# Kernel optimization log

Measured on AMD Instinct MI355X. Metric: run time of the kernel, lower is better.

The kernel has to match this reference:

```python
import jax, jax.numpy as jnp
import numpy as np

B, H, SQ, SKV, D = 2, 16, 2048, 3072, 64
NUM_PT = 1024  # SKV = NUM_PT + SQ


def setup_inputs() -> dict:
    key = jax.random.key(0)
    kq, kk, kv = jax.random.split(key, 3)
    q = jax.random.normal(kq, (B, H, SQ, D), dtype=jnp.float32)
    k = jax.random.normal(kk, (B, H, SKV, D), dtype=jnp.float32)
    v = jax.random.normal(kv, (B, H, SKV, D), dtype=jnp.float32)
    return {"q": q, "k": k, "v": v, "num_pt": NUM_PT}


def _prefix_causal_mask(sq, skv, num_pt):
    # kv_idx < num_pt always visible (global prefix); otherwise causal on
    # shifted index: q_idx >= kv_idx - num_pt
    q_idx = jnp.arange(sq)[:, None]   # [SQ,1]
    kv_idx = jnp.arange(skv)[None, :]  # [1,SKV]
    return (kv_idx < num_pt) | (q_idx >= kv_idx - num_pt)  # [SQ,SKV]


def reference(q, k, v, num_pt):
    scale = 1.0 / jnp.sqrt(jnp.asarray(q.shape[-1], q.dtype))
    # [B,H,SQ,SKV]
    scores = jnp.einsum("bhqd,bhkd->bhqk", q, k) * scale
    mask = _prefix_causal_mask(q.shape[2], k.shape[2], num_pt)  # [SQ,SKV]
    neg = jnp.asarray(jnp.finfo(scores.dtype).min, scores.dtype)
    scores = jnp.where(mask[None, None], scores, neg)
    probs = jax.nn.softmax(scores, axis=-1)
    return jnp.einsum("bhqk,bhkd->bhqd", probs, v)
```

## Files before the change

### kernel.cpp

```cpp
#include <hip/hip_runtime.h>

#define B_ 2
#define H_ 16
#define SQ_ 2048
#define SKV_ 3072
#define DH 64
#define QT 128
#define KVT 64
#define LDK 72

typedef __attribute__((ext_vector_type(4))) float f32x4;
typedef __attribute__((ext_vector_type(8))) short bf16x8;

__device__ __forceinline__ unsigned pk2(float a, float b) {
  return __builtin_amdgcn_perm(__float_as_uint(b) + 0x8000u,
                               __float_as_uint(a) + 0x8000u, 0x07060302u);
}

__global__ __launch_bounds__(512, 4) void attn_fwd(
    const float* __restrict__ qg_, const float* __restrict__ kg_,
    const float* __restrict__ vg_, const int* __restrict__ num_pt_p,
    float* __restrict__ og_) {
  __shared__ __align__(16) short Ks[2][KVT][LDK];
  __shared__ __align__(16) short Vt[2][DH][LDK];
  __shared__ __align__(16) short Ps[8][16][LDK];

  const int tid  = (int)threadIdx.x;
  const int lane = tid & 63;
  const int w    = tid >> 6;
  const int lq   = lane & 15;
  const int quad = lane >> 4;
  const int x    = (int)blockIdx.x;
  const int y    = (int)blockIdx.y;
  const int qb   = (y & 16) ? x : (15 - x);
  const int num_pt = *num_pt_p;
  const int q0   = qb * QT;

  const float* qg = qg_ + (size_t)y * SQ_ * DH;
  const float* kg = kg_ + (size_t)y * SKV_ * DH;
  const float* vg = vg_ + (size_t)y * SKV_ * DH;
  float*       og = og_ + (size_t)y * SQ_ * DH;

  const float SC = 0.125f * 1.44269504088896341f;

  const int qrow = q0 + w * 16 + lq;
  bf16x8 qf[2];
  {
    const float* qp = qg + (size_t)qrow * DH + quad * 8;
#pragma unroll
    for (int kh = 0; kh < 2; ++kh) {
      float4 a = *(const float4*)(qp + kh * 32);
      float4 b = *(const float4*)(qp + kh * 32 + 4);
      union { unsigned u[4]; bf16x8 hh; } t;
      t.u[0] = pk2(a.x * SC, a.y * SC);
      t.u[1] = pk2(a.z * SC, a.w * SC);
      t.u[2] = pk2(b.x * SC, b.y * SC);
      t.u[3] = pk2(b.z * SC, b.w * SC);
      qf[kh] = t.hh;
    }
  }

  f32x4 O[4];
#pragma unroll
  for (int i = 0; i < 4; ++i) O[i] = (f32x4){0.f, 0.f, 0.f, 0.f};
  f32x4 l4 = (f32x4){0.f, 0.f, 0.f, 0.f};

  int n_tiles = (q0 + QT - 1 + num_pt) / KVT + 1;
  if (n_tiles > SKV_ / KVT) n_tiles = SKV_ / KVT;

  const int krow = tid >> 3;
  const int kcol = (tid & 7) * 8;
  const int vp   = tid & 31;
  const int vd0  = (tid >> 5) * 4;
  const float* kQp = kg + (size_t)krow * DH + kcol;
  const float* vQp = vg + (size_t)(2 * vp) * DH + vd0;

  float4 kf0 = *(const float4*)(kQp);
  float4 kf1 = *(const float4*)(kQp + 4);
  float4 vfa = *(const float4*)(vQp);
  float4 vfb = *(const float4*)(vQp + DH);

  {
    union { unsigned u[4]; bf16x8 hh; } tk;
    tk.u[0] = pk2(kf0.x, kf0.y);
    tk.u[1] = pk2(kf0.z, kf0.w);
    tk.u[2] = pk2(kf1.x, kf1.y);
    tk.u[3] = pk2(kf1.z, kf1.w);
    *(bf16x8*)&Ks[0][krow][kcol] = tk.hh;
    *(unsigned*)&Vt[0][vd0 + 0][2 * vp] = pk2(vfa.x, vfb.x);
    *(unsigned*)&Vt[0][vd0 + 1][2 * vp] = pk2(vfa.y, vfb.y);
    *(unsigned*)&Vt[0][vd0 + 2][2 * vp] = pk2(vfa.z, vfb.z);
    *(unsigned*)&Vt[0][vd0 + 3][2 * vp] = pk2(vfa.w, vfb.w);
  }
  __syncthreads();

  const int lim = qrow + num_pt;

  for (int t = 0; t < n_tiles; ++t) {
    const int kb = t * KVT;
    const int buf = t & 1;
    const bool more = (t + 1 < n_tiles);

    if (more) {
      const size_t nb = (size_t)(t + 1) * KVT * DH;
      kf0 = *(const float4*)(kQp + nb);
      kf1 = *(const float4*)(kQp + nb + 4);
      vfa = *(const float4*)(vQp + nb);
      vfb = *(const float4*)(vQp + nb + DH);
    }

    f32x4 st[4];
#pragma unroll
    for (int mg = 0; mg < 4; ++mg) {
      bf16x8 ka0 = *(const bf16x8*)&Ks[buf][mg * 16 + lq][quad * 8];
      bf16x8 ka1 = *(const bf16x8*)&Ks[buf][mg * 16 + lq][32 + quad * 8];
      f32x4 c = (f32x4){0.f, 0.f, 0.f, 0.f};
      c = __builtin_amdgcn_mfma_f32_16x16x32_bf16(ka0, qf[0], c, 0, 0, 0);
      c = __builtin_amdgcn_mfma_f32_16x16x32_bf16(ka1, qf[1], c, 0, 0, 0);
      st[mg] = c;
    }

    if (kb + KVT - 1 > q0 + w * 16 + num_pt) {
#pragma unroll
      for (int mg = 0; mg < 4; ++mg)
#pragma unroll
        for (int r = 0; r < 4; ++r)
          if (kb + mg * 16 + quad * 4 + r > lim) st[mg][r] = -__builtin_inff();
    }

#pragma unroll
    for (int mg = 0; mg < 4; ++mg)
#pragma unroll
      for (int r = 0; r < 4; ++r) {
        float pe = __builtin_amdgcn_exp2f(st[mg][r]);
        st[mg][r] = pe;
        l4[r] += pe;
      }

#pragma unroll
    for (int mg = 0; mg < 4; ++mg) {
      *(uint2*)&Ps[w][lq][mg * 16 + quad * 4] =
          make_uint2(pk2(st[mg][0], st[mg][1]), pk2(st[mg][2], st[mg][3]));
    }
    bf16x8 pa0 = *(const bf16x8*)&Ps[w][lq][quad * 8];
    bf16x8 pa1 = *(const bf16x8*)&Ps[w][lq][32 + quad * 8];
#pragma unroll
    for (int dg = 0; dg < 4; ++dg) {
      bf16x8 vb0 = *(const bf16x8*)&Vt[buf][dg * 16 + lq][quad * 8];
      bf16x8 vb1 = *(const bf16x8*)&Vt[buf][dg * 16 + lq][32 + quad * 8];
      O[dg] = __builtin_amdgcn_mfma_f32_16x16x32_bf16(vb0, pa0, O[dg], 0, 0, 0);
      O[dg] = __builtin_amdgcn_mfma_f32_16x16x32_bf16(vb1, pa1, O[dg], 0, 0, 0);
    }

    if (more) {
      union { unsigned u[4]; bf16x8 hh; } tk;
      tk.u[0] = pk2(kf0.x, kf0.y);
      tk.u[1] = pk2(kf0.z, kf0.w);
      tk.u[2] = pk2(kf1.x, kf1.y);
      tk.u[3] = pk2(kf1.z, kf1.w);
      *(bf16x8*)&Ks[buf ^ 1][krow][kcol] = tk.hh;
      *(unsigned*)&Vt[buf ^ 1][vd0 + 0][2 * vp] = pk2(vfa.x, vfb.x);
      *(unsigned*)&Vt[buf ^ 1][vd0 + 1][2 * vp] = pk2(vfa.y, vfb.y);
      *(unsigned*)&Vt[buf ^ 1][vd0 + 2][2 * vp] = pk2(vfa.z, vfb.z);
      *(unsigned*)&Vt[buf ^ 1][vd0 + 3][2 * vp] = pk2(vfa.w, vfb.w);
    }
    __syncthreads();
  }

  float l_run = l4[0] + l4[1] + l4[2] + l4[3];
  l_run += __shfl_xor(l_run, 16);
  l_run += __shfl_xor(l_run, 32);
  float inv = 1.0f / l_run;
  float* op = og + (size_t)qrow * DH + quad * 4;
#pragma unroll
  for (int dg = 0; dg < 4; ++dg) {
    float4 o4;
    o4.x = O[dg][0] * inv;
    o4.y = O[dg][1] * inv;
    o4.z = O[dg][2] * inv;
    o4.w = O[dg][3] * inv;
    *(float4*)(op + dg * 16) = o4;
  }
}

extern "C" void kernel_launch(void* const* d_in, const int* in_sizes, int n_in,
                              void* d_out, int out_size, void* d_ws, size_t ws_size,
                              hipStream_t stream) {
  const float* q = (const float*)d_in[0];
  const float* k = (const float*)d_in[1];
  const float* v = (const float*)d_in[2];
  const int* np  = (const int*)d_in[3];
  float* out = (float*)d_out;
  dim3 grid(SQ_ / QT, B_ * H_);
  attn_fwd<<<grid, dim3(512), 0, stream>>>(q, k, v, np, out);
}
```

Before: 157.7 us.

## Prepack K and transposed V to bf16 in workspace, read fragments directly

Adds a prepass kernel that converts K to bf16 and V to a transposed bf16 layout in the workspace. A new attention kernel with 64-row query tiles and 256 threads loads MFMA fragments straight from global memory into registers, prefetching the next K tile. This removes the LDS staging and the per-tile barriers. It costs an extra kernel launch and a full K/V read and write pass, and it falls back to the old kernel when the workspace is too small.

```diff
diff --git a/kernel.cpp b/kernel.cpp
--- a/kernel.cpp
+++ b/kernel.cpp
@@ -5,7 +5,6 @@
 #define SQ_ 2048
 #define SKV_ 3072
 #define DH 64
-#define QT 128
 #define KVT 64
 #define LDK 72
 
@@ -17,6 +16,189 @@
                                __float_as_uint(a) + 0x8000u, 0x07060302u);
 }
 
+__global__ __launch_bounds__(256) void prepack(
+    const float* __restrict__ kg, const float* __restrict__ vg,
+    short* __restrict__ kb, short* __restrict__ vtb) {
+  const int t = (int)threadIdx.x;
+  const int x = (int)blockIdx.x;
+  const int y = (int)blockIdx.y;
+  if (blockIdx.z == 0) {
+    const float* src = kg + ((size_t)y * SKV_ + (size_t)x * 64) * DH;
+    short* dst = kb + ((size_t)y * SKV_ + (size_t)x * 64) * DH;
+#pragma unroll
+    for (int i = 0; i < 4; ++i) {
+      size_t off = (size_t)i * 1024 + t * 4;
+      float4 f = *(const float4*)(src + off);
+      *(uint2*)(dst + off) = make_uint2(pk2(f.x, f.y), pk2(f.z, f.w));
+    }
+  } else {
+    __shared__ __align__(16) short L[DH][LDK];
+    const float* src = vg + ((size_t)y * SKV_ + (size_t)x * 64) * DH;
+    const int vp = t & 31;
+    const int d0 = (t >> 5) * 8;
+    float4 a0 = *(const float4*)(src + (size_t)(2 * vp) * DH + d0);
+    float4 a1 = *(const float4*)(src + (size_t)(2 * vp) * DH + d0 + 4);
+    float4 b0 = *(const float4*)(src + (size_t)(2 * vp + 1) * DH + d0);
+    float4 b1 = *(const float4*)(src + (size_t)(2 * vp + 1) * DH + d0 + 4);
+    *(unsigned*)&L[d0 + 0][2 * vp] = pk2(a0.x, b0.x);
+    *(unsigned*)&L[d0 + 1][2 * vp] = pk2(a0.y, b0.y);
+    *(unsigned*)&L[d0 + 2][2 * vp] = pk2(a0.z, b0.z);
+    *(unsigned*)&L[d0 + 3][2 * vp] = pk2(a0.w, b0.w);
+    *(unsigned*)&L[d0 + 4][2 * vp] = pk2(a1.x, b1.x);
+    *(unsigned*)&L[d0 + 5][2 * vp] = pk2(a1.y, b1.y);
+    *(unsigned*)&L[d0 + 6][2 * vp] = pk2(a1.z, b1.z);
+    *(unsigned*)&L[d0 + 7][2 * vp] = pk2(a1.w, b1.w);
+    __syncthreads();
+#pragma unroll
+    for (int i = 0; i < 2; ++i) {
+      int cid = t + i * 256;
+      int d = cid >> 3, c = cid & 7;
+      *(bf16x8*)(vtb + ((size_t)y * DH + d) * SKV_ + (size_t)x * 64 + c * 8) =
+          *(const bf16x8*)&L[d][c * 8];
+    }
+  }
+}
+
+__global__ __launch_bounds__(256, 4) void attn_fwd2(
+    const short* __restrict__ kb_, const short* __restrict__ vtb_,
+    const float* __restrict__ qg_, const int* __restrict__ num_pt_p,
+    float* __restrict__ og_) {
+  __shared__ __align__(16) short Ps[4][16][LDK];
+
+  const int tid  = (int)threadIdx.x;
+  const int lane = tid & 63;
+  const int w    = tid >> 6;
+  const int lq   = lane & 15;
+  const int quad = lane >> 4;
+  const int x    = (int)blockIdx.x;
+  const int y    = (int)blockIdx.y;
+  const int g = y >> 3;
+  const int xr = (x + ((g & 2) ? 8 : 0)) & 31;
+  const int qb = (g & 1) ? (31 - xr) : xr;
+  const int num_pt = *num_pt_p;
+  const int q0 = qb * 64;
+
+  const short* Kb = kb_ + (size_t)y * SKV_ * DH;
+  const short* Vb = vtb_ + (size_t)y * DH * SKV_;
+  const float* qg = qg_ + (size_t)y * SQ_ * DH;
+  float*       og = og_ + (size_t)y * SQ_ * DH;
+
+  const float SC = 0.125f * 1.44269504088896341f;
+
+  const int qrow = q0 + w * 16 + lq;
+  bf16x8 qf[2];
+  {
+    const float* qp = qg + (size_t)qrow * DH + quad * 8;
+#pragma unroll
+    for (int kh = 0; kh < 2; ++kh) {
+      float4 a = *(const float4*)(qp + kh * 32);
+      float4 b = *(const float4*)(qp + kh * 32 + 4);
+      union { unsigned u[4]; bf16x8 hh; } t;
+      t.u[0] = pk2(a.x * SC, a.y * SC);
+      t.u[1] = pk2(a.z * SC, a.w * SC);
+      t.u[2] = pk2(b.x * SC, b.y * SC);
+      t.u[3] = pk2(b.z * SC, b.w * SC);
+      qf[kh] = t.hh;
+    }
+  }
+
+  f32x4 O[4];
+#pragma unroll
+  for (int i = 0; i < 4; ++i) O[i] = (f32x4){0.f, 0.f, 0.f, 0.f};
+  f32x4 l4 = (f32x4){0.f, 0.f, 0.f, 0.f};
+
+  int nw = (q0 + w * 16 + 15 + num_pt) / KVT + 1;
+  if (nw > SKV_ / KVT) nw = SKV_ / KVT;
+  const int lim = qrow + num_pt;
+
+  const short* kA = Kb + (size_t)lq * DH + quad * 8;
+  const short* vA = Vb + (size_t)lq * SKV_ + quad * 8;
+
+  bf16x8 ka[4][2];
+#pragma unroll
+  for (int mg = 0; mg < 4; ++mg) {
+    ka[mg][0] = *(const bf16x8*)(kA + (size_t)(mg * 16) * DH);
+    ka[mg][1] = *(const bf16x8*)(kA + (size_t)(mg * 16) * DH + 32);
+  }
+
+  for (int t = 0; t < nw; ++t) {
+    const int kb = t * KVT;
+    const bool more = (t + 1 < nw);
+
+    bf16x8 vb[4][2];
+#pragma unroll
+    for (int dg = 0; dg < 4; ++dg) {
+      const short* vp = vA + (size_t)(dg * 16) * SKV_ + kb;
+      vb[dg][0] = *(const bf16x8*)(vp);
+      vb[dg][1] = *(const bf16x8*)(vp + 32);
+    }
+
+    f32x4 st[4];
+#pragma unroll
+    for (int mg = 0; mg < 4; ++mg) {
+      f32x4 c = (f32x4){0.f, 0.f, 0.f, 0.f};
+      c = __builtin_amdgcn_mfma_f32_16x16x32_bf16(ka[mg][0], qf[0], c, 0, 0, 0);
+      c = __builtin_amdgcn_mfma_f32_16x16x32_bf16(ka[mg][1], qf[1], c, 0, 0, 0);
+      st[mg] = c;
+    }
+
+    if (more) {
+      const short* kp = kA + (size_t)(kb + KVT) * DH;
+#pragma unroll
+      for (int mg = 0; mg < 4; ++mg) {
+        ka[mg][0] = *(const bf16x8*)(kp + (size_t)(mg * 16) * DH);
+        ka[mg][1] = *(const bf16x8*)(kp + (size_t)(mg * 16) * DH + 32);
+      }
+    }
+
+    if (kb + KVT - 1 > q0 + w * 16 + num_pt) {
+#pragma unroll
+      for (int mg = 0; mg < 4; ++mg)
+#pragma unroll
+        for (int r = 0; r < 4; ++r)
+          if (kb + mg * 16 + quad * 4 + r > lim) st[mg][r] = -__builtin_inff();
+    }
+
+#pragma unroll
+    for (int mg = 0; mg < 4; ++mg)
+#pragma unroll
+      for (int r = 0; r < 4; ++r) {
+        float pe = __builtin_amdgcn_exp2f(st[mg][r]);
+        st[mg][r] = pe;
+        l4[r] += pe;
+      }
+
+#pragma unroll
+    for (int mg = 0; mg < 4; ++mg) {
+      *(uint2*)&Ps[w][lq][mg * 16 + quad * 4] =
+          make_uint2(pk2(st[mg][0], st[mg][1]), pk2(st[mg][2], st[mg][3]));
+    }
+    bf16x8 pa0 = *(const bf16x8*)&Ps[w][lq][quad * 8];
+    bf16x8 pa1 = *(const bf16x8*)&Ps[w][lq][32 + quad * 8];
+#pragma unroll
+    for (int dg = 0; dg < 4; ++dg) {
+      O[dg] = __builtin_amdgcn_mfma_f32_16x16x32_bf16(vb[dg][0], pa0, O[dg], 0, 0, 0);
+      O[dg] = __builtin_amdgcn_mfma_f32_16x16x32_bf16(vb[dg][1], pa1, O[dg], 0, 0, 0);
+    }
+  }
+
+  float l_run = l4[0] + l4[1] + l4[2] + l4[3];
+  l_run += __shfl_xor(l_run, 16);
+  l_run += __shfl_xor(l_run, 32);
+  float inv = 1.0f / l_run;
+  float* op = og + (size_t)qrow * DH + quad * 4;
+#pragma unroll
+  for (int dg = 0; dg < 4; ++dg) {
+    float4 o4;
+    o4.x = O[dg][0] * inv;
+    o4.y = O[dg][1] * inv;
+    o4.z = O[dg][2] * inv;
+    o4.w = O[dg][3] * inv;
+    *(float4*)(op + dg * 16) = o4;
+  }
+}
+
+#define QT7 128
 __global__ __launch_bounds__(512, 4) void attn_fwd(
     const float* __restrict__ qg_, const float* __restrict__ kg_,
     const float* __restrict__ vg_, const int* __restrict__ num_pt_p,
@@ -24,7 +206,6 @@
   __shared__ __align__(16) short Ks[2][KVT][LDK];
   __shared__ __align__(16) short Vt[2][DH][LDK];
   __shared__ __align__(16) short Ps[8][16][LDK];
-
   const int tid  = (int)threadIdx.x;
   const int lane = tid & 63;
   const int w    = tid >> 6;
@@ -34,15 +215,12 @@
   const int y    = (int)blockIdx.y;
   const int qb   = (y & 16) ? x : (15 - x);
   const int num_pt = *num_pt_p;
-  const int q0   = qb * QT;
-
+  const int q0   = qb * QT7;
   const float* qg = qg_ + (size_t)y * SQ_ * DH;
   const float* kg = kg_ + (size_t)y * SKV_ * DH;
   const float* vg = vg_ + (size_t)y * SKV_ * DH;
   float*       og = og_ + (size_t)y * SQ_ * DH;
-
   const float SC = 0.125f * 1.44269504088896341f;
-
   const int qrow = q0 + w * 16 + lq;
   bf16x8 qf[2];
   {
@@ -59,33 +237,26 @@
       qf[kh] = t.hh;
     }
   }
-
   f32x4 O[4];
 #pragma unroll
   for (int i = 0; i < 4; ++i) O[i] = (f32x4){0.f, 0.f, 0.f, 0.f};
   f32x4 l4 = (f32x4){0.f, 0.f, 0.f, 0.f};
-
-  int n_tiles = (q0 + QT - 1 + num_pt) / KVT + 1;
+  int n_tiles = (q0 + QT7 - 1 + num_pt) / KVT + 1;
   if (n_tiles > SKV_ / KVT) n_tiles = SKV_ / KVT;
-
   const int krow = tid >> 3;
   const int kcol = (tid & 7) * 8;
   const int vp   = tid & 31;
   const int vd0  = (tid >> 5) * 4;
   const float* kQp = kg + (size_t)krow * DH + kcol;
   const float* vQp = vg + (size_t)(2 * vp) * DH + vd0;
-
   float4 kf0 = *(const float4*)(kQp);
   float4 kf1 = *(const float4*)(kQp + 4);
   float4 vfa = *(const float4*)(vQp);
   float4 vfb = *(const float4*)(vQp + DH);
-
   {
     union { unsigned u[4]; bf16x8 hh; } tk;
-    tk.u[0] = pk2(kf0.x, kf0.y);
-    tk.u[1] = pk2(kf0.z, kf0.w);
-    tk.u[2] = pk2(kf1.x, kf1.y);
-    tk.u[3] = pk2(kf1.z, kf1.w);
+    tk.u[0] = pk2(kf0.x, kf0.y); tk.u[1] = pk2(kf0.z, kf0.w);
+    tk.u[2] = pk2(kf1.x, kf1.y); tk.u[3] = pk2(kf1.z, kf1.w);
     *(bf16x8*)&Ks[0][krow][kcol] = tk.hh;
     *(unsigned*)&Vt[0][vd0 + 0][2 * vp] = pk2(vfa.x, vfb.x);
     *(unsigned*)&Vt[0][vd0 + 1][2 * vp] = pk2(vfa.y, vfb.y);
@@ -93,14 +264,11 @@
     *(unsigned*)&Vt[0][vd0 + 3][2 * vp] = pk2(vfa.w, vfb.w);
   }
   __syncthreads();
-
   const int lim = qrow + num_pt;
-
   for (int t = 0; t < n_tiles; ++t) {
     const int kb = t * KVT;
     const int buf = t & 1;
     const bool more = (t + 1 < n_tiles);
-
     if (more) {
       const size_t nb = (size_t)(t + 1) * KVT * DH;
       kf0 = *(const float4*)(kQp + nb);
@@ -108,7 +276,6 @@
       vfa = *(const float4*)(vQp + nb);
       vfb = *(const float4*)(vQp + nb + DH);
     }
-
     f32x4 st[4];
 #pragma unroll
     for (int mg = 0; mg < 4; ++mg) {
@@ -119,7 +286,6 @@
       c = __builtin_amdgcn_mfma_f32_16x16x32_bf16(ka1, qf[1], c, 0, 0, 0);
       st[mg] = c;
     }
-
     if (kb + KVT - 1 > q0 + w * 16 + num_pt) {
 #pragma unroll
       for (int mg = 0; mg < 4; ++mg)
@@ -127,7 +293,6 @@
         for (int r = 0; r < 4; ++r)
           if (kb + mg * 16 + quad * 4 + r > lim) st[mg][r] = -__builtin_inff();
     }
-
 #pragma unroll
     for (int mg = 0; mg < 4; ++mg)
 #pragma unroll
@@ -136,7 +301,6 @@
         st[mg][r] = pe;
         l4[r] += pe;
       }
-
 #pragma unroll
     for (int mg = 0; mg < 4; ++mg) {
       *(uint2*)&Ps[w][lq][mg * 16 + quad * 4] =
@@ -151,13 +315,10 @@
       O[dg] = __builtin_amdgcn_mfma_f32_16x16x32_bf16(vb0, pa0, O[dg], 0, 0, 0);
       O[dg] = __builtin_amdgcn_mfma_f32_16x16x32_bf16(vb1, pa1, O[dg], 0, 0, 0);
     }
-
     if (more) {
       union { unsigned u[4]; bf16x8 hh; } tk;
-      tk.u[0] = pk2(kf0.x, kf0.y);
-      tk.u[1] = pk2(kf0.z, kf0.w);
-      tk.u[2] = pk2(kf1.x, kf1.y);
-      tk.u[3] = pk2(kf1.z, kf1.w);
+      tk.u[0] = pk2(kf0.x, kf0.y); tk.u[1] = pk2(kf0.z, kf0.w);
+      tk.u[2] = pk2(kf1.x, kf1.y); tk.u[3] = pk2(kf1.z, kf1.w);
       *(bf16x8*)&Ks[buf ^ 1][krow][kcol] = tk.hh;
       *(unsigned*)&Vt[buf ^ 1][vd0 + 0][2 * vp] = pk2(vfa.x, vfb.x);
       *(unsigned*)&Vt[buf ^ 1][vd0 + 1][2 * vp] = pk2(vfa.y, vfb.y);
@@ -166,7 +327,6 @@
     }
     __syncthreads();
   }
-
   float l_run = l4[0] + l4[1] + l4[2] + l4[3];
   l_run += __shfl_xor(l_run, 16);
   l_run += __shfl_xor(l_run, 32);
@@ -191,6 +351,14 @@
   const float* v = (const float*)d_in[2];
   const int* np  = (const int*)d_in[3];
   float* out = (float*)d_out;
-  dim3 grid(SQ_ / QT, B_ * H_);
-  attn_fwd<<<grid, dim3(512), 0, stream>>>(q, k, v, np, out);
-}
+  const size_t kv_elems = (size_t)B_ * H_ * SKV_ * DH;
+  const size_t need = 2 * kv_elems * sizeof(short);
+  if (ws_size >= need) {
+    short* kb  = (short*)d_ws;
+    short* vtb = kb + kv_elems;
+    prepack<<<dim3(SKV_ / 64, B_ * H_, 2), dim3(256), 0, stream>>>(k, v, kb, vtb);
+    attn_fwd2<<<dim3(32, B_ * H_), dim3(256), 0, stream>>>(kb, vtb, q, np, out);
+  } else {
+    attn_fwd<<<dim3(16, B_ * H_), dim3(512), 0, stream>>>(q, k, v, np, out);
+  }
+}
```

Result: slower. 329.7 us (+109.1%).

## Switch attention to 32x32x16 MFMA with 4 waves of 32 query rows

Applied to the files above, without the earlier changes.

Replaces the 16x16x32 bf16 MFMA tiles with 32x32x16 ones, so each of 4 waves (256 threads) handles 32 query rows instead of 8 waves handling 16. Each thread now loads twice as much K/V data per tile, and a per-wave skip is added for KV tiles that lie entirely beyond the causal limit. The aim is higher MFMA efficiency per LDS read and less redundant K/V fragment loading across waves. In exchange, fewer waves per block and more registers per thread may reduce latency hiding, and the change to launch bounds lowers the occupancy hint.

```diff
diff --git a/kernel.cpp b/kernel.cpp
--- a/kernel.cpp
+++ b/kernel.cpp
@@ -9,7 +9,7 @@
 #define KVT 64
 #define LDK 72
 
-typedef __attribute__((ext_vector_type(4))) float f32x4;
+typedef __attribute__((ext_vector_type(16))) float f32x16;
 typedef __attribute__((ext_vector_type(8))) short bf16x8;
 
 __device__ __forceinline__ unsigned pk2(float a, float b) {
@@ -17,19 +17,19 @@
                                __float_as_uint(a) + 0x8000u, 0x07060302u);
 }
 
-__global__ __launch_bounds__(512, 4) void attn_fwd(
+__global__ __launch_bounds__(256, 2) void attn_fwd(
     const float* __restrict__ qg_, const float* __restrict__ kg_,
     const float* __restrict__ vg_, const int* __restrict__ num_pt_p,
     float* __restrict__ og_) {
   __shared__ __align__(16) short Ks[2][KVT][LDK];
   __shared__ __align__(16) short Vt[2][DH][LDK];
-  __shared__ __align__(16) short Ps[8][16][LDK];
+  __shared__ __align__(16) short Ps[4][32][LDK];
 
   const int tid  = (int)threadIdx.x;
   const int lane = tid & 63;
   const int w    = tid >> 6;
-  const int lq   = lane & 15;
-  const int quad = lane >> 4;
+  const int n    = lane & 31;
+  const int h    = lane >> 5;
   const int x    = (int)blockIdx.x;
   const int y    = (int)blockIdx.y;
   const int qb   = (y & 16) ? x : (15 - x);
@@ -43,58 +43,66 @@
 
   const float SC = 0.125f * 1.44269504088896341f;
 
-  const int qrow = q0 + w * 16 + lq;
-  bf16x8 qf[2];
+  const int qrow = q0 + w * 32 + n;
+  bf16x8 qf[4];
   {
-    const float* qp = qg + (size_t)qrow * DH + quad * 8;
-#pragma unroll
-    for (int kh = 0; kh < 2; ++kh) {
-      float4 a = *(const float4*)(qp + kh * 32);
-      float4 b = *(const float4*)(qp + kh * 32 + 4);
+    const float* qp = qg + (size_t)qrow * DH + h * 8;
+#pragma unroll
+    for (int ks = 0; ks < 4; ++ks) {
+      float4 a = *(const float4*)(qp + ks * 16);
+      float4 b = *(const float4*)(qp + ks * 16 + 4);
       union { unsigned u[4]; bf16x8 hh; } t;
       t.u[0] = pk2(a.x * SC, a.y * SC);
       t.u[1] = pk2(a.z * SC, a.w * SC);
       t.u[2] = pk2(b.x * SC, b.y * SC);
       t.u[3] = pk2(b.z * SC, b.w * SC);
-      qf[kh] = t.hh;
+      qf[ks] = t.hh;
     }
   }
 
-  f32x4 O[4];
-#pragma unroll
-  for (int i = 0; i < 4; ++i) O[i] = (f32x4){0.f, 0.f, 0.f, 0.f};
-  f32x4 l4 = (f32x4){0.f, 0.f, 0.f, 0.f};
+  f32x16 O[2];
+  O[0] = (f32x16)(0.f);
+  O[1] = (f32x16)(0.f);
+  float l4[4] = {0.f, 0.f, 0.f, 0.f};
 
   int n_tiles = (q0 + QT - 1 + num_pt) / KVT + 1;
   if (n_tiles > SKV_ / KVT) n_tiles = SKV_ / KVT;
-
-  const int krow = tid >> 3;
-  const int kcol = (tid & 7) * 8;
+  const int wave_last = q0 + w * 32 + 31 + num_pt;
+  const int lim = qrow + num_pt;
+
+  const int krow = tid >> 2;
+  const int kcol = (tid & 3) * 16;
   const int vp   = tid & 31;
-  const int vd0  = (tid >> 5) * 4;
+  const int vd0  = (tid >> 5) * 8;
   const float* kQp = kg + (size_t)krow * DH + kcol;
   const float* vQp = vg + (size_t)(2 * vp) * DH + vd0;
 
-  float4 kf0 = *(const float4*)(kQp);
-  float4 kf1 = *(const float4*)(kQp + 4);
-  float4 vfa = *(const float4*)(vQp);
-  float4 vfb = *(const float4*)(vQp + DH);
+  float4 kf[4], va0, va1, vb0, vb1;
+#pragma unroll
+  for (int i = 0; i < 4; ++i) kf[i] = *(const float4*)(kQp + i * 4);
+  va0 = *(const float4*)(vQp);
+  va1 = *(const float4*)(vQp + 4);
+  vb0 = *(const float4*)(vQp + DH);
+  vb1 = *(const float4*)(vQp + DH + 4);
 
   {
-    union { unsigned u[4]; bf16x8 hh; } tk;
-    tk.u[0] = pk2(kf0.x, kf0.y);
-    tk.u[1] = pk2(kf0.z, kf0.w);
-    tk.u[2] = pk2(kf1.x, kf1.y);
-    tk.u[3] = pk2(kf1.z, kf1.w);
-    *(bf16x8*)&Ks[0][krow][kcol] = tk.hh;
-    *(unsigned*)&Vt[0][vd0 + 0][2 * vp] = pk2(vfa.x, vfb.x);
-    *(unsigned*)&Vt[0][vd0 + 1][2 * vp] = pk2(vfa.y, vfb.y);
-    *(unsigned*)&Vt[0][vd0 + 2][2 * vp] = pk2(vfa.z, vfb.z);
-    *(unsigned*)&Vt[0][vd0 + 3][2 * vp] = pk2(vfa.w, vfb.w);
+    union { unsigned u[4]; bf16x8 hh; } t0, t1;
+    t0.u[0] = pk2(kf[0].x, kf[0].y); t0.u[1] = pk2(kf[0].z, kf[0].w);
+    t0.u[2] = pk2(kf[1].x, kf[1].y); t0.u[3] = pk2(kf[1].z, kf[1].w);
+    t1.u[0] = pk2(kf[2].x, kf[2].y); t1.u[1] = pk2(kf[2].z, kf[2].w);
+    t1.u[2] = pk2(kf[3].x, kf[3].y); t1.u[3] = pk2(kf[3].z, kf[3].w);
+    *(bf16x8*)&Ks[0][krow][kcol] = t0.hh;
+    *(bf16x8*)&Ks[0][krow][kcol + 8] = t1.hh;
+    *(unsigned*)&Vt[0][vd0 + 0][2 * vp] = pk2(va0.x, vb0.x);
+    *(unsigned*)&Vt[0][vd0 + 1][2 * vp] = pk2(va0.y, vb0.y);
+    *(unsigned*)&Vt[0][vd0 + 2][2 * vp] = pk2(va0.z, vb0.z);
+    *(unsigned*)&Vt[0][vd0 + 3][2 * vp] = pk2(va0.w, vb0.w);
+    *(unsigned*)&Vt[0][vd0 + 4][2 * vp] = pk2(va1.x, vb1.x);
+    *(unsigned*)&Vt[0][vd0 + 5][2 * vp] = pk2(va1.y, vb1.y);
+    *(unsigned*)&Vt[0][vd0 + 6][2 * vp] = pk2(va1.z, vb1.z);
+    *(unsigned*)&Vt[0][vd0 + 7][2 * vp] = pk2(va1.w, vb1.w);
   }
   __syncthreads();
-
-  const int lim = qrow + num_pt;
 
   for (int t = 0; t < n_tiles; ++t) {
     const int kb = t * KVT;
@@ -103,84 +111,104 @@
 
     if (more) {
       const size_t nb = (size_t)(t + 1) * KVT * DH;
-      kf0 = *(const float4*)(kQp + nb);
-      kf1 = *(const float4*)(kQp + nb + 4);
-      vfa = *(const float4*)(vQp + nb);
-      vfb = *(const float4*)(vQp + nb + DH);
-    }
-
-    f32x4 st[4];
-#pragma unroll
-    for (int mg = 0; mg < 4; ++mg) {
-      bf16x8 ka0 = *(const bf16x8*)&Ks[buf][mg * 16 + lq][quad * 8];
-      bf16x8 ka1 = *(const bf16x8*)&Ks[buf][mg * 16 + lq][32 + quad * 8];
-      f32x4 c = (f32x4){0.f, 0.f, 0.f, 0.f};
-      c = __builtin_amdgcn_mfma_f32_16x16x32_bf16(ka0, qf[0], c, 0, 0, 0);
-      c = __builtin_amdgcn_mfma_f32_16x16x32_bf16(ka1, qf[1], c, 0, 0, 0);
-      st[mg] = c;
-    }
-
-    if (kb + KVT - 1 > q0 + w * 16 + num_pt) {
-#pragma unroll
-      for (int mg = 0; mg < 4; ++mg)
-#pragma unroll
-        for (int r = 0; r < 4; ++r)
-          if (kb + mg * 16 + quad * 4 + r > lim) st[mg][r] = -__builtin_inff();
-    }
-
-#pragma unroll
-    for (int mg = 0; mg < 4; ++mg)
-#pragma unroll
-      for (int r = 0; r < 4; ++r) {
-        float pe = __builtin_amdgcn_exp2f(st[mg][r]);
-        st[mg][r] = pe;
-        l4[r] += pe;
+#pragma unroll
+      for (int i = 0; i < 4; ++i) kf[i] = *(const float4*)(kQp + nb + i * 4);
+      va0 = *(const float4*)(vQp + nb);
+      va1 = *(const float4*)(vQp + nb + 4);
+      vb0 = *(const float4*)(vQp + nb + DH);
+      vb1 = *(const float4*)(vQp + nb + DH + 4);
+    }
+
+    if (kb <= wave_last) {
+      f32x16 st[2];
+#pragma unroll
+      for (int mg = 0; mg < 2; ++mg) {
+        f32x16 c = (f32x16)(0.f);
+#pragma unroll
+        for (int ks = 0; ks < 4; ++ks) {
+          bf16x8 ka = *(const bf16x8*)&Ks[buf][mg * 32 + n][ks * 16 + h * 8];
+          c = __builtin_amdgcn_mfma_f32_32x32x16_bf16(ka, qf[ks], c, 0, 0, 0);
+        }
+        st[mg] = c;
       }
 
-#pragma unroll
-    for (int mg = 0; mg < 4; ++mg) {
-      *(uint2*)&Ps[w][lq][mg * 16 + quad * 4] =
-          make_uint2(pk2(st[mg][0], st[mg][1]), pk2(st[mg][2], st[mg][3]));
-    }
-    bf16x8 pa0 = *(const bf16x8*)&Ps[w][lq][quad * 8];
-    bf16x8 pa1 = *(const bf16x8*)&Ps[w][lq][32 + quad * 8];
-#pragma unroll
-    for (int dg = 0; dg < 4; ++dg) {
-      bf16x8 vb0 = *(const bf16x8*)&Vt[buf][dg * 16 + lq][quad * 8];
-      bf16x8 vb1 = *(const bf16x8*)&Vt[buf][dg * 16 + lq][32 + quad * 8];
-      O[dg] = __builtin_amdgcn_mfma_f32_16x16x32_bf16(vb0, pa0, O[dg], 0, 0, 0);
-      O[dg] = __builtin_amdgcn_mfma_f32_16x16x32_bf16(vb1, pa1, O[dg], 0, 0, 0);
+      if (kb + KVT - 1 > q0 + w * 32 + num_pt) {
+#pragma unroll
+        for (int mg = 0; mg < 2; ++mg)
+#pragma unroll
+          for (int r = 0; r < 16; ++r) {
+            int kv = kb + mg * 32 + (r & 3) + 8 * (r >> 2) + 4 * h;
+            if (kv > lim) st[mg][r] = -__builtin_inff();
+          }
+      }
+
+#pragma unroll
+      for (int mg = 0; mg < 2; ++mg)
+#pragma unroll
+        for (int r = 0; r < 16; ++r) {
+          float pe = __builtin_amdgcn_exp2f(st[mg][r]);
+          st[mg][r] = pe;
+          l4[r & 3] += pe;
+        }
+
+#pragma unroll
+      for (int mg = 0; mg < 2; ++mg)
+#pragma unroll
+        for (int r = 0; r < 4; ++r) {
+          *(uint2*)&Ps[w][n][mg * 32 + r * 8 + 4 * h] =
+              make_uint2(pk2(st[mg][r * 4 + 0], st[mg][r * 4 + 1]),
+                         pk2(st[mg][r * 4 + 2], st[mg][r * 4 + 3]));
+        }
+      bf16x8 pb[4];
+#pragma unroll
+      for (int ks = 0; ks < 4; ++ks)
+        pb[ks] = *(const bf16x8*)&Ps[w][n][ks * 16 + h * 8];
+
+#pragma unroll
+      for (int dg = 0; dg < 2; ++dg) {
+#pragma unroll
+        for (int ks = 0; ks < 4; ++ks) {
+          bf16x8 va = *(const bf16x8*)&Vt[buf][dg * 32 + n][ks * 16 + h * 8];
+          O[dg] = __builtin_amdgcn_mfma_f32_32x32x16_bf16(va, pb[ks], O[dg], 0, 0, 0);
+        }
+      }
     }
 
     if (more) {
-      union { unsigned u[4]; bf16x8 hh; } tk;
-      tk.u[0] = pk2(kf0.x, kf0.y);
-      tk.u[1] = pk2(kf0.z, kf0.w);
-      tk.u[2] = pk2(kf1.x, kf1.y);
-      tk.u[3] = pk2(kf1.z, kf1.w);
-      *(bf16x8*)&Ks[buf ^ 1][krow][kcol] = tk.hh;
-      *(unsigned*)&Vt[buf ^ 1][vd0 + 0][2 * vp] = pk2(vfa.x, vfb.x);
-      *(unsigned*)&Vt[buf ^ 1][vd0 + 1][2 * vp] = pk2(vfa.y, vfb.y);
-      *(unsigned*)&Vt[buf ^ 1][vd0 + 2][2 * vp] = pk2(vfa.z, vfb.z);
-      *(unsigned*)&Vt[buf ^ 1][vd0 + 3][2 * vp] = pk2(vfa.w, vfb.w);
+      union { unsigned u[4]; bf16x8 hh; } t0, t1;
+      t0.u[0] = pk2(kf[0].x, kf[0].y); t0.u[1] = pk2(kf[0].z, kf[0].w);
+      t0.u[2] = pk2(kf[1].x, kf[1].y); t0.u[3] = pk2(kf[1].z, kf[1].w);
+      t1.u[0] = pk2(kf[2].x, kf[2].y); t1.u[1] = pk2(kf[2].z, kf[2].w);
+      t1.u[2] = pk2(kf[3].x, kf[3].y); t1.u[3] = pk2(kf[3].z, kf[3].w);
+      *(bf16x8*)&Ks[buf ^ 1][krow][kcol] = t0.hh;
+      *(bf16x8*)&Ks[buf ^ 1][krow][kcol + 8] = t1.hh;
+      *(unsigned*)&Vt[buf ^ 1][vd0 + 0][2 * vp] = pk2(va0.x, vb0.x);
+      *(unsigned*)&Vt[buf ^ 1][vd0 + 1][2 * vp] = pk2(va0.y, vb0.y);
+      *(unsigned*)&Vt[buf ^ 1][vd0 + 2][2 * vp] = pk2(va0.z, vb0.z);
+      *(unsigned*)&Vt[buf ^ 1][vd0 + 3][2 * vp] = pk2(va0.w, vb0.w);
+      *(unsigned*)&Vt[buf ^ 1][vd0 + 4][2 * vp] = pk2(va1.x, vb1.x);
+      *(unsigned*)&Vt[buf ^ 1][vd0 + 5][2 * vp] = pk2(va1.y, vb1.y);
+      *(unsigned*)&Vt[buf ^ 1][vd0 + 6][2 * vp] = pk2(va1.z, vb1.z);
+      *(unsigned*)&Vt[buf ^ 1][vd0 + 7][2 * vp] = pk2(va1.w, vb1.w);
     }
     __syncthreads();
   }
 
-  float l_run = l4[0] + l4[1] + l4[2] + l4[3];
-  l_run += __shfl_xor(l_run, 16);
+  float l_run = (l4[0] + l4[1]) + (l4[2] + l4[3]);
   l_run += __shfl_xor(l_run, 32);
   float inv = 1.0f / l_run;
-  float* op = og + (size_t)qrow * DH + quad * 4;
-#pragma unroll
-  for (int dg = 0; dg < 4; ++dg) {
-    float4 o4;
-    o4.x = O[dg][0] * inv;
-    o4.y = O[dg][1] * inv;
-    o4.z = O[dg][2] * inv;
-    o4.w = O[dg][3] * inv;
-    *(float4*)(op + dg * 16) = o4;
-  }
+  float* op = og + (size_t)qrow * DH + 4 * h;
+#pragma unroll
+  for (int dg = 0; dg < 2; ++dg)
+#pragma unroll
+    for (int r = 0; r < 4; ++r) {
+      float4 o4;
+      o4.x = O[dg][r * 4 + 0] * inv;
+      o4.y = O[dg][r * 4 + 1] * inv;
+      o4.z = O[dg][r * 4 + 2] * inv;
+      o4.w = O[dg][r * 4 + 3] * inv;
+      *(float4*)(op + dg * 32 + r * 8) = o4;
+    }
 }
 
 extern "C" void kernel_launch(void* const* d_in, const int* in_sizes, int n_in,
@@ -192,5 +220,5 @@
   const int* np  = (const int*)d_in[3];
   float* out = (float*)d_out;
   dim3 grid(SQ_ / QT, B_ * H_);
-  attn_fwd<<<grid, dim3(512), 0, stream>>>(q, k, v, np, out);
+  attn_fwd<<<grid, dim3(256), 0, stream>>>(q, k, v, np, out);
 }
```

Measured after the change: 170.3 us. +8.0%, slower.
